# Kernel tuning notes

Hardware: AMD Instinct MI355X
Metric: run time of the kernel (lower is better)

The kernel has to match this reference:

```python
import jax, jax.numpy as jnp
import numpy as np

H = 64
L = 3
NG = 1024
# node types: 0 user, 1 card, 2 transaction, 3 merchant, 4 location, 5 device
N_NODES = [100000, 150000, 500000, 20000, 5000, 50000]
N_TX = N_NODES[2]
FEAT_DIMS = [8, 6, 12, 6, 5, 5]
NAMES = ["user", "card", "transaction", "merchant", "location", "device"]
# relation r -> (src_type, dst_type); order matches the HeteroConv dict:
# owns, made, at, in, using, followed_by, owned_by, made_with, receives, has, used_in, preceded
REL = [(0, 1), (1, 2), (2, 3), (2, 4), (2, 5), (2, 2), (1, 0), (2, 1), (3, 2), (4, 2), (5, 2), (2, 2)]
E_CNT = [150000, 500000, 500000, 500000, 500000, 500000, 150000, 500000, 500000, 500000, 500000, 500000]


def gat_conv(x_src, x_dst, src, dst, W, a_s, a_d, b, n_dst):
    # PyG GATConv, heads=1, shared src/dst linear (int in_channels), no self-loops (bipartite hetero)
    xs = x_src @ W  # [Ns, H]
    xd = x_dst @ W  # [Nd, H]
    e = jax.nn.leaky_relu((xs @ a_s)[src] + (xd @ a_d)[dst], 0.2)  # [E]
    m = jax.ops.segment_max(e, dst, num_segments=n_dst)
    m = jnp.where(jnp.isfinite(m), m, 0.0)
    p = jnp.exp(e - m[dst])
    s = jax.ops.segment_sum(p, dst, num_segments=n_dst)
    alpha = p / (s[dst] + 1e-16)
    out = jax.ops.segment_sum(alpha[:, None] * xs[src], dst, num_segments=n_dst)
    return out + b


def setup_inputs():
    key = jax.random.key(0)
    ks = iter(jax.random.split(key, 80))
    inp = {}
    for n, d, nm in zip(N_NODES, FEAT_DIMS, NAMES):
        inp["x_" + nm] = jax.random.normal(next(ks), (n, d), jnp.float32)
    for d, nm in zip(FEAT_DIMS, NAMES):
        inp["emb_" + nm + "_W"] = (jax.random.normal(next(ks), (d, H), jnp.float32) / np.sqrt(d)).astype(jnp.float32)
        inp["emb_" + nm + "_b"] = jnp.zeros((H,), jnp.float32)
    inp["gat_W"] = (jax.random.normal(next(ks), (L, 12, H, H), jnp.float32) / np.sqrt(H)).astype(jnp.float32)
    inp["gat_a_src"] = jax.random.normal(next(ks), (L, 12, H), jnp.float32) * 0.1
    inp["gat_a_dst"] = jax.random.normal(next(ks), (L, 12, H), jnp.float32) * 0.1
    inp["gat_b"] = jnp.zeros((L, 12, H), jnp.float32)
    inp["pool_W"] = (jax.random.normal(next(ks), (2 * H, H), jnp.float32) / np.sqrt(2 * H)).astype(jnp.float32)
    inp["pool_b"] = jnp.zeros((H,), jnp.float32)
    inp["cls_W1"] = (jax.random.normal(next(ks), (H, H), jnp.float32) / np.sqrt(H)).astype(jnp.float32)
    inp["cls_b1"] = jnp.zeros((H,), jnp.float32)
    inp["cls_W2"] = (jax.random.normal(next(ks), (H, 1), jnp.float32) / np.sqrt(H)).astype(jnp.float32)
    inp["cls_b2"] = jnp.zeros((1,), jnp.float32)
    for r, (s, d) in enumerate(REL):
        inp[f"e{r}_src"] = jax.random.randint(next(ks), (E_CNT[r],), 0, N_NODES[s])
        inp[f"e{r}_dst"] = jax.random.randint(next(ks), (E_CNT[r],), 0, N_NODES[d])
    inp["batch"] = jnp.sort(jax.random.randint(next(ks), (N_TX,), 0, NG))
    return inp


def reference(x_user, x_card, x_transaction, x_merchant, x_location, x_device,
              emb_user_W, emb_user_b, emb_card_W, emb_card_b,
              emb_transaction_W, emb_transaction_b, emb_merchant_W, emb_merchant_b,
              emb_location_W, emb_location_b, emb_device_W, emb_device_b,
              gat_W, gat_a_src, gat_a_dst, gat_b,
              pool_W, pool_b, cls_W1, cls_b1, cls_W2, cls_b2,
              e0_src, e0_dst, e1_src, e1_dst, e2_src, e2_dst, e3_src, e3_dst,
              e4_src, e4_dst, e5_src, e5_dst, e6_src, e6_dst, e7_src, e7_dst,
              e8_src, e8_dst, e9_src, e9_dst, e10_src, e10_dst, e11_src, e11_dst,
              batch):
    edges = [(e0_src, e0_dst), (e1_src, e1_dst), (e2_src, e2_dst), (e3_src, e3_dst),
             (e4_src, e4_dst), (e5_src, e5_dst), (e6_src, e6_dst), (e7_src, e7_dst),
             (e8_src, e8_dst), (e9_src, e9_dst), (e10_src, e10_dst), (e11_src, e11_dst)]
    x = [x_user @ emb_user_W + emb_user_b,
         x_card @ emb_card_W + emb_card_b,
         x_transaction @ emb_transaction_W + emb_transaction_b,
         x_merchant @ emb_merchant_W + emb_merchant_b,
         x_location @ emb_location_W + emb_location_b,
         x_device @ emb_device_W + emb_device_b]
    for l in range(L):
        agg = [jnp.zeros((n, H), x[0].dtype) for n in N_NODES]
        for r, (s, d) in enumerate(REL):  # HeteroConv default aggr='sum'
            agg[d] = agg[d] + gat_conv(x[s], x[d], edges[r][0], edges[r][1],
                                       gat_W[l, r], gat_a_src[l, r], gat_a_dst[l, r],
                                       gat_b[l, r], N_NODES[d])
        x = [jax.nn.relu(a) for a in agg]  # dropout(p=0.2) is identity in eval mode
    tx = x[2]
    cnt = jax.ops.segment_sum(jnp.ones((N_TX,), tx.dtype), batch, num_segments=NG)
    mean_pool = jax.ops.segment_sum(tx, batch, num_segments=NG) / jnp.maximum(cnt, 1.0)[:, None]
    max_pool = jax.ops.segment_max(tx, batch, num_segments=NG)
    max_pool = jnp.where(jnp.isfinite(max_pool), max_pool, 0.0)
    pooled = jnp.concatenate([mean_pool, max_pool], axis=1) @ pool_W + pool_b
    h = jax.nn.relu(tx @ cls_W1 + cls_b1)
    fraud_scores = jax.nn.sigmoid(h @ cls_W2 + cls_b2)
    return fraud_scores, pooled
```

## Files before the change

kernel.cpp:

```cpp
#include <hip/hip_runtime.h>
#include <hip/hip_bf16.h>

typedef unsigned int u32;
typedef unsigned short u16;
typedef _Float16 f16;
typedef float f32x4 __attribute__((ext_vector_type(4)));
typedef short bf16x8 __attribute__((ext_vector_type(8)));

#define CDIV(a,b) (((a)+(b)-1)/(b))

__device__ __forceinline__ float bf2f(u32 h){ return __uint_as_float(h<<16); }
__device__ __forceinline__ u16 f2bf(float f){
  u32 u=__float_as_uint(f);
  return (u16)((u + 0x7fffu + ((u>>16)&1u))>>16);
}
__device__ __forceinline__ u32 fenc(float f){
  u32 u=__float_as_uint(f);
  return (u&0x80000000u)?~u:(u|0x80000000u);
}
__device__ __forceinline__ float fdec2(u32 e){
  u32 u=(e&0x80000000u)?(e&0x7fffffffu):~e;
  return __uint_as_float(u);
}
__device__ __forceinline__ void unpack8(const u16* p, float* xr){
  uint4 v=*(const uint4*)p;
  xr[0]=bf2f(v.x&0xffffu); xr[1]=bf2f(v.x>>16);
  xr[2]=bf2f(v.y&0xffffu); xr[3]=bf2f(v.y>>16);
  xr[4]=bf2f(v.z&0xffffu); xr[5]=bf2f(v.z>>16);
  xr[6]=bf2f(v.w&0xffffu); xr[7]=bf2f(v.w>>16);
}
__device__ __forceinline__ int iclamp(int i, int n){
  unsigned u=(unsigned)i; return (u>=(unsigned)n)?0:i;
}

struct EdgeTab {
  const int* dst[12];
  const int* src[12];
  int seo[13];
  int rpo[13];
  int nd[12];
  int ns[12];
};

struct GTab {
  int nn[6]; int xo[6];
  int rst[12]; int rdt[12];
  int aso[12], ado[12], rpo[12], seo[12];
  int tord[6]; int bofs[7];
  int abofs[7];
  int nrel[6], rel[6][6];
  int nrole[6]; int rwv[6][12]; int rofs[6][12];
  int dszb;
};

__global__ void kdiag(float* out, int n, float v){
  int i=blockIdx.x*blockDim.x+threadIdx.x;
  if(i<n) out[i]=(i==0)?v:0.f;
}
__global__ void kzeroi(int* p, int n){
  int i=blockIdx.x*blockDim.x+threadIdx.x;
  if(i<n) p[i]=0;
}
__global__ void kbsum(const float* __restrict__ gb, float* __restrict__ bsum){
  int l=blockIdx.x/6, t=blockIdx.x%6, j=threadIdx.x;
  const int rd[12]={1,2,3,4,5,2,0,1,2,2,2,2};
  float a=0.f;
  #pragma unroll
  for(int r=0;r<12;++r) if(rd[r]==t) a += gb[(l*12+r)*64 + j];
  bsum[(l*6+t)*64 + j]=a;
}
__global__ void kwconv(const float* __restrict__ gw, u16* __restrict__ wt, int total){
  int o=blockIdx.x*blockDim.x+threadIdx.x;
  if(o>=total) return;
  int m=o>>12, rem=o&4095, j=rem>>6, k=rem&63;
  wt[o]=f2bf(gw[(m<<12)+(k<<6)+j]);
}
__global__ void kwv(const float* __restrict__ gw, const float* __restrict__ gas,
                    const float* __restrict__ gad, float* __restrict__ wv){
  int m=blockIdx.x;
  int lr=m>>1, role=m&1;
  int k=threadIdx.x;
  const float* a=(role?gad:gas)+(size_t)lr*64;
  const float* W=gw+(size_t)lr*4096;
  float acc=0.f;
  for(int j=0;j<64;++j) acc += W[k*64+j]*a[j];
  wv[(size_t)m*64+k]=acc;
}

__global__ void khistC(EdgeTab et, int* __restrict__ RP, int Etot, int c0, int c1){
  int i=blockIdx.x*blockDim.x+threadIdx.x;
  if(i>=Etot) return;
  int r=0;
  #pragma unroll
  for(int k=1;k<12;++k) r += (i>=et.seo[k]) ? 1 : 0;
  int e=i-et.seo[r];
  int rpidx=et.rpo[r]+iclamp(et.dst[r][e], et.nd[r]);
  if(rpidx>=c0 && rpidx<c1) atomicAdd(RP+rpidx,1);
}
__global__ void kscan1(const int* __restrict__ hist, int* __restrict__ rp, int* __restrict__ bsum, int N){
  __shared__ int lds[256];
  __shared__ int pref[256];
  int b=blockIdx.x, t=threadIdx.x;
  int base=b*4096+t*16;
  int v[16]; int s=0;
  #pragma unroll
  for(int k=0;k<16;++k){ int idx=base+k; v[k]=(idx<N)?hist[idx]:0; s+=v[k]; }
  lds[t]=s; __syncthreads();
  if(t==0){ int run=0; for(int i=0;i<256;++i){ pref[i]=run; run+=lds[i]; } bsum[b]=run; }
  __syncthreads();
  int run=pref[t];
  #pragma unroll
  for(int k=0;k<16;++k){ int idx=base+k; if(idx<N) rp[idx]=run; run+=v[k]; }
}
__global__ void kscan2b(int* bsum, int nb){
  __shared__ int lds[256], pref[256], tot;
  int t=threadIdx.x;
  int v[4]; int s=0;
  #pragma unroll
  for(int k=0;k<4;++k){ int idx=t*4+k; v[k]=(idx<nb)?bsum[idx]:0; s+=v[k]; }
  lds[t]=s; __syncthreads();
  if(t==0){ int run=0; for(int i=0;i<256;++i){ pref[i]=run; run+=lds[i]; } tot=run; }
  __syncthreads();
  int run=pref[t];
  #pragma unroll
  for(int k=0;k<4;++k){ int idx=t*4+k; if(idx<nb){ int x=v[k]; bsum[idx]=run; run+=x; } }
  if(t==0) bsum[nb]=tot;
}
__global__ void kscan3(int* __restrict__ rp, const int* __restrict__ bsum, int N){
  int i=blockIdx.x*blockDim.x+threadIdx.x;
  if(i<N) rp[i]+=bsum[i>>12];
}
__global__ void kscatterC(EdgeTab et, int* __restrict__ RP, int* __restrict__ SRCS,
                          int Etot, int c0, int c1){
  int i=blockIdx.x*blockDim.x+threadIdx.x;
  if(i>=Etot) return;
  int r=0;
  #pragma unroll
  for(int k=1;k<12;++k) r += (i>=et.seo[k]) ? 1 : 0;
  int e=i-et.seo[r];
  int rpidx=et.rpo[r]+iclamp(et.dst[r][e], et.nd[r]);
  if(rpidx>=c0 && rpidx<c1){
    int pos=atomicAdd(RP+rpidx,1);
    SRCS[pos]=iclamp(et.src[r][e], et.ns[r]);
  }
}

template<int D>
__global__ void kemb(const float* __restrict__ xin, const float* __restrict__ W,
                     const float* __restrict__ b, u16* __restrict__ xout, int N,
                     const float* __restrict__ WV0, f16* __restrict__ AA, GTab tab, int t){
  int n=blockIdx.x*blockDim.x+threadIdx.x;
  if(n>=N) return;
  float xr[D];
  #pragma unroll
  for(int k=0;k<D;++k) xr[k]=xin[(long)n*D+k];
  float o[64];
  u16* orow=xout+(long)n*64;
  #pragma unroll
  for(int j0=0;j0<64;j0+=8){
    #pragma unroll
    for(int jj=0;jj<8;++jj){
      float a=b[j0+jj];
      #pragma unroll
      for(int k=0;k<D;++k) a += xr[k]*W[k*64+j0+jj];
      o[j0+jj]=a;
    }
    uint4 pk;
    pk.x=(u32)f2bf(o[j0+0])|((u32)f2bf(o[j0+1])<<16);
    pk.y=(u32)f2bf(o[j0+2])|((u32)f2bf(o[j0+3])<<16);
    pk.z=(u32)f2bf(o[j0+4])|((u32)f2bf(o[j0+5])<<16);
    pk.w=(u32)f2bf(o[j0+6])|((u32)f2bf(o[j0+7])<<16);
    *(uint4*)(orow+j0)=pk;
  }
  int nr=tab.nrole[t];
  for(int ro=0;ro<nr;++ro){
    const float* wv=WV0+(size_t)tab.rwv[t][ro]*64;
    float acc=0.f;
    #pragma unroll
    for(int k=0;k<64;++k) acc += o[k]*wv[k];
    AA[tab.rofs[t][ro]+n]=(f16)acc;
  }
}

__global__ void kalphaM(const u16* __restrict__ X, const float* __restrict__ WVl,
                        f16* __restrict__ AA, GTab tab){
  __shared__ float wv[12*64];
  int b=blockIdx.x, tid=threadIdx.x;
  int ti=0;
  #pragma unroll
  for(int k=1;k<6;++k) ti += (b>=tab.abofs[k]) ? 1 : 0;
  int t=tab.tord[ti];
  int nr=tab.nrole[t];
  for(int i=tid;i<nr*64;i+=256){
    int ro=i>>6, j=i&63;
    wv[i]=WVl[tab.rwv[t][ro]*64+j];
  }
  __syncthreads();
  int nid=(b-tab.abofs[ti])*256+tid;
  if(nid>=tab.nn[t]) return;
  const u16* row=X+((long)tab.xo[t]+nid)*64;
  float xr[64];
  #pragma unroll
  for(int j=0;j<64;j+=8) unpack8(row+j,xr+j);
  for(int ro=0;ro<nr;++ro){
    float acc=0.f;
    #pragma unroll
    for(int k=0;k<64;++k) acc += xr[k]*wv[ro*64+k];
    AA[tab.rofs[t][ro]+nid]=(f16)acc;
  }
}

__global__ void kmg(const f16* __restrict__ AA, u32* __restrict__ MGl, GTab tab){
  const int NB=8;
  int b=blockIdx.x;
  int ro=b/NB, part=b%NB;
  int r=ro>>1, role=ro&1;
  int base,len;
  if(role==0){ base=tab.aso[r];           len=tab.nn[tab.rst[r]]; }
  else       { base=tab.dszb+tab.ado[r];  len=tab.nn[tab.rdt[r]]; }
  int i0=(int)((long)len*part/NB), i1=(int)((long)len*(part+1)/NB);
  float m=-3.4e38f;
  for(int i=i0+threadIdx.x;i<i1;i+=256) m=fmaxf(m,(float)AA[base+i]);
  #pragma unroll
  for(int off=32;off;off>>=1) m=fmaxf(m,__shfl_xor(m,off));
  __shared__ float red[4];
  if((threadIdx.x&63)==0) red[threadIdx.x>>6]=m;
  __syncthreads();
  if(threadIdx.x==0){
    float mm=fmaxf(fmaxf(red[0],red[1]),fmaxf(red[2],red[3]));
    atomicMax(MGl+ro,fenc(mm));
  }
}

#define LZ 0
#define LW 8192
__global__ void kfusedM2(const u16* __restrict__ Xc, u16* __restrict__ Xn,
                         const u16* __restrict__ WTl, const f16* __restrict__ AA,
                         const int* __restrict__ RP, const int* __restrict__ SRCS,
                         const float* __restrict__ BSl, const u32* __restrict__ MGl,
                         GTab tab){
  __shared__ char L[16384];
  int tid=threadIdx.x;
  int b=blockIdx.x;
  int ti=0;
  #pragma unroll
  for(int k=1;k<6;++k) ti += (b>=tab.bofs[k]) ? 1 : 0;
  int t=tab.tord[ti];
  int d0=(b-tab.bofs[ti])*64;
  int Nt=tab.nn[t];
  int nid=tid>>2, q=tid&3;
  int d=d0+nid;

  f32x4 acc[4];
  #pragma unroll
  for(int ct=0;ct<4;++ct){ acc[ct][0]=0.f; acc[ct][1]=0.f; acc[ct][2]=0.f; acc[ct][3]=0.f; }

  int nrel=tab.nrel[t];
  for(int ri=0;ri<nrel;++ri){
    int r=tab.rel[t][ri];
    float msum=fdec2(MGl[r*2])+fdec2(MGl[r*2+1]);
    float m = msum>=0.f? msum : 0.2f*msum;
    __syncthreads();
    {
      const uint4* s4=(const uint4*)(WTl+(size_t)r*4096);
      uint4 v0=s4[tid*2], v1=s4[tid*2+1];
      int b0=tid*32, j=b0>>7;
      *(uint4*)(L+LW+((b0   )^((j&7)<<4)))=v0;
      *(uint4*)(L+LW+((b0+16)^((j&7)<<4)))=v1;
    }
    float z[16];
    #pragma unroll
    for(int k=0;k<16;++k) z[k]=0.f;
    float sden=0.f;
    if(d<Nt){
      int b1=RP[tab.rpo[r]+d];
      int b0e= d? RP[tab.rpo[r]+d-1] : tab.seo[r];
      float adv=(float)AA[tab.dszb+tab.ado[r]+d];
      const u16* xbase=Xc+(long)tab.xo[tab.rst[r]]*64;
      const f16* asp=AA+tab.aso[r];
      int e=b0e;
      for(; e+1<b1; e+=2){
        int sr0=SRCS[e], sr1=SRCS[e+1];
        float ev0=(float)asp[sr0]+adv; ev0 = ev0>=0.f?ev0:0.2f*ev0;
        float ev1=(float)asp[sr1]+adv; ev1 = ev1>=0.f?ev1:0.2f*ev1;
        float p0=__expf(ev0-m), p1=__expf(ev1-m);
        const u16* rw0=xbase+(long)sr0*64+q*16;
        const u16* rw1=xbase+(long)sr1*64+q*16;
        uint4 a0=*(const uint4*)rw0;
        uint4 a1=*(const uint4*)(rw0+8);
        uint4 c0=*(const uint4*)rw1;
        uint4 c1=*(const uint4*)(rw1+8);
        sden+=p0+p1;
        float xr[8];
        unpack8((const u16*)&a0,xr);
        #pragma unroll
        for(int k=0;k<8;++k) z[k]+=p0*xr[k];
        unpack8((const u16*)&a1,xr);
        #pragma unroll
        for(int k=0;k<8;++k) z[8+k]+=p0*xr[k];
        unpack8((const u16*)&c0,xr);
        #pragma unroll
        for(int k=0;k<8;++k) z[k]+=p1*xr[k];
        unpack8((const u16*)&c1,xr);
        #pragma unroll
        for(int k=0;k<8;++k) z[8+k]+=p1*xr[k];
      }
      if(e<b1){
        int sr0=SRCS[e];
        float ev0=(float)asp[sr0]+adv; ev0 = ev0>=0.f?ev0:0.2f*ev0;
        float p0=__expf(ev0-m);
        const u16* rw0=xbase+(long)sr0*64+q*16;
        uint4 a0=*(const uint4*)rw0;
        uint4 a1=*(const uint4*)(rw0+8);
        sden+=p0;
        float xr[8];
        unpack8((const u16*)&a0,xr);
        #pragma unroll
        for(int k=0;k<8;++k) z[k]+=p0*xr[k];
        unpack8((const u16*)&a1,xr);
        #pragma unroll
        for(int k=0;k<8;++k) z[8+k]+=p0*xr[k];
      }
    }
    float inv=1.f/(sden+1e-16f);
    {
      uint4 p0,p1;
      p0.x=(u32)f2bf(z[0]*inv) |((u32)f2bf(z[1]*inv)<<16);
      p0.y=(u32)f2bf(z[2]*inv) |((u32)f2bf(z[3]*inv)<<16);
      p0.z=(u32)f2bf(z[4]*inv) |((u32)f2bf(z[5]*inv)<<16);
      p0.w=(u32)f2bf(z[6]*inv) |((u32)f2bf(z[7]*inv)<<16);
      p1.x=(u32)f2bf(z[8]*inv) |((u32)f2bf(z[9]*inv)<<16);
      p1.y=(u32)f2bf(z[10]*inv)|((u32)f2bf(z[11]*inv)<<16);
      p1.z=(u32)f2bf(z[12]*inv)|((u32)f2bf(z[13]*inv)<<16);
      p1.w=(u32)f2bf(z[14]*inv)|((u32)f2bf(z[15]*inv)<<16);
      int zb=nid*128+q*32;
      *(uint4*)(L+LZ+((zb   )^((nid&7)<<4)))=p0;
      *(uint4*)(L+LZ+((zb+16)^((nid&7)<<4)))=p1;
    }
    __syncthreads();
    {
      int w=tid>>6, l=tid&63;
      int nt=w*16;
      int arow=nt+(l&15);
      int kb=(l>>4)*8;
      #pragma unroll
      for(int ks=0;ks<64;ks+=32){
        int ab=arow*128+(ks+kb)*2;
        uint4 av=*(uint4*)(L+LZ+(ab^((arow&7)<<4)));
        bf16x8 af=*(bf16x8*)&av;
        #pragma unroll
        for(int ct=0;ct<4;++ct){
          int jrow=ct*16+(l&15);
          int bb=jrow*128+(ks+kb)*2;
          uint4 bv=*(uint4*)(L+LW+(bb^((jrow&7)<<4)));
          bf16x8 bfr=*(bf16x8*)&bv;
          acc[ct]=__builtin_amdgcn_mfma_f32_16x16x32_bf16(af,bfr,acc[ct],0,0,0);
        }
      }
    }
  }
  __syncthreads();
  {
    int w=tid>>6, l=tid&63;
    int nt=w*16;
    #pragma unroll
    for(int ct=0;ct<4;++ct){
      #pragma unroll
      for(int r4=0;r4<4;++r4){
        int crow=nt+(l>>4)*4+r4;
        int ccol=ct*16+(l&15);
        int cb=crow*256+ccol*4;
        *(float*)(L+(cb^((crow&7)<<4)))=acc[ct][r4];
      }
    }
  }
  __syncthreads();
  {
    int nn=tid>>2, cq=tid&3;
    if(d0+nn<Nt){
      float cv[16];
      #pragma unroll
      for(int p=0;p<4;++p){
        int cb=nn*256+cq*64+p*16;
        uint4 v=*(uint4*)(L+(cb^((nn&7)<<4)));
        const float* f=(const float*)&v;
        cv[p*4+0]=f[0]; cv[p*4+1]=f[1]; cv[p*4+2]=f[2]; cv[p*4+3]=f[3];
      }
      const float* bs=BSl+t*64+cq*16;
      u32 wd[8];
      #pragma unroll
      for(int i=0;i<8;++i){
        float lo=fmaxf(cv[2*i]  +bs[2*i],  0.f);
        float hi=fmaxf(cv[2*i+1]+bs[2*i+1],0.f);
        wd[i]=(u32)f2bf(lo)|((u32)f2bf(hi)<<16);
      }
      u16* orow=Xn+((long)tab.xo[t]+d0+nn)*64+cq*16;
      uint4 s0; s0.x=wd[0]; s0.y=wd[1]; s0.z=wd[2]; s0.w=wd[3];
      uint4 s1; s1.x=wd[4]; s1.y=wd[5]; s1.z=wd[6]; s1.w=wd[7];
      *(uint4*)orow=s0;
      *(uint4*)(orow+8)=s1;
    }
  }
}

__global__ void kcls(const u16* __restrict__ tx, const float* __restrict__ W1,
                     const float* __restrict__ b1, const float* __restrict__ W2,
                     const float* __restrict__ b2, float* __restrict__ out, int N){
  int n=blockIdx.x*blockDim.x+threadIdx.x;
  if(n>=N) return;
  const u16* row=tx+(long)n*64;
  float xr[64];
  #pragma unroll
  for(int j=0;j<64;j+=8) unpack8(row+j,xr+j);
  float acc2=0.f;
  for(int j=0;j<64;++j){
    float a=b1[j];
    #pragma unroll
    for(int k=0;k<64;++k) a += xr[k]*W1[k*64+j];
    a=fmaxf(a,0.f);
    acc2 += a*W2[j];
  }
  float zv=acc2+b2[0];
  out[n]=1.f/(1.f+__expf(-zv));
}

__global__ void kgrp(const int* __restrict__ batch, int* __restrict__ grp, int N){
  int g=blockIdx.x*blockDim.x+threadIdx.x;
  if(g>1024) return;
  if(g==1024){ grp[1024]=N; return; }
  int lo=0, hi=N;
  while(lo<hi){ int mid=(lo+hi)>>1; if(batch[mid]<g) lo=mid+1; else hi=mid; }
  grp[g]=lo;
}
__global__ void kpoolf(const u16* __restrict__ tx, const int* __restrict__ grp,
                       const float* __restrict__ pW, const float* __restrict__ pb,
                       float* __restrict__ out){
  __shared__ float S[256], M[256], V[128];
  int g=blockIdx.x, t=threadIdx.x, w=t>>6, j=t&63;
  int n0=grp[g], n1=grp[g+1];
  float s=0.f, m=-3.4e38f;
  for(int n=n0+w; n<n1; n+=4){
    float v=bf2f(tx[(long)n*64+j]);
    s+=v; m=fmaxf(m,v);
  }
  S[t]=s; M[t]=m; __syncthreads();
  if(t<64){
    float ss=S[t]+S[t+64]+S[t+128]+S[t+192];
    float mm=fmaxf(fmaxf(M[t],M[t+64]),fmaxf(M[t+128],M[t+192]));
    int cnt=n1-n0;
    V[t]=ss/fmaxf((float)cnt,1.f);
    V[64+t]=(cnt>0)?mm:0.f;
  }
  __syncthreads();
  if(t<64){
    float acc=pb[t];
    for(int k=0;k<128;++k) acc+=V[k]*pW[k*64+t];
    out[(long)g*64+t]=acc;
  }
}

extern "C" void kernel_launch(void* const* d_in, const int* in_sizes, int n_in,
                              void* d_out, int out_size, void* d_ws, size_t ws_size,
                              hipStream_t stream){
  const int   NN[6]={100000,150000,500000,20000,5000,50000};
  const long  XO[6]={0,100000,250000,750000,770000,775000};
  const int   RS[12]={0,1,2,2,2,2,1,2,3,4,5,2};
  const int   RD[12]={1,2,3,4,5,2,0,1,2,2,2,2};
  const int   EC[12]={150000,500000,500000,500000,500000,500000,150000,500000,500000,500000,500000,500000};

  const float* xin[6];  for(int t=0;t<6;++t) xin[t]=(const float*)d_in[t];
  const float* embW[6]; const float* embB[6];
  for(int t=0;t<6;++t){ embW[t]=(const float*)d_in[6+2*t]; embB[t]=(const float*)d_in[7+2*t]; }
  const float* gatW =(const float*)d_in[18];
  const float* gatAs=(const float*)d_in[19];
  const float* gatAd=(const float*)d_in[20];
  const float* gatB =(const float*)d_in[21];
  const float* poolW=(const float*)d_in[22];
  const float* poolB=(const float*)d_in[23];
  const float* W1=(const float*)d_in[24];
  const float* b1=(const float*)d_in[25];
  const float* W2=(const float*)d_in[26];
  const float* b2=(const float*)d_in[27];
  const int* esrc[12]; const int* edst[12];
  for(int r=0;r<12;++r){ esrc[r]=(const int*)d_in[28+2*r]; edst[r]=(const int*)d_in[29+2*r]; }
  const int* batch=(const int*)d_in[52];
  float* out=(float*)d_out;
  (void)in_sizes; (void)n_in;

  EdgeTab et;
  GTab tab;
  int rpo=0, seo=0, asz=0, dsz=0;
  for(int r=0;r<12;++r){
    et.dst[r]=edst[r]; et.src[r]=esrc[r];
    et.seo[r]=seo; et.rpo[r]=rpo;
    et.nd[r]=NN[RD[r]]; et.ns[r]=NN[RS[r]];
    tab.rst[r]=RS[r]; tab.rdt[r]=RD[r];
    tab.seo[r]=seo; tab.rpo[r]=rpo;
    tab.aso[r]=asz; tab.ado[r]=dsz;
    seo+=EC[r]; rpo+=NN[RD[r]]+1;
    asz+=NN[RS[r]]; dsz+=NN[RD[r]];
  }
  et.seo[12]=seo; et.rpo[12]=rpo;
  const int Etot=seo;
  const int RPtot=rpo;
  tab.dszb=asz;
  for(int t=0;t<6;++t){ tab.nn[t]=NN[t]; tab.xo[t]=(int)XO[t]; }
  const int TORD[6]={4,3,5,2,1,0};
  int bo=0, abo=0;
  for(int i=0;i<6;++i){
    int t=TORD[i];
    tab.tord[i]=t;
    tab.bofs[i]=bo;   bo+=CDIV(NN[t],64);
    tab.abofs[i]=abo; abo+=CDIV(NN[t],256);
  }
  tab.bofs[6]=bo; tab.abofs[6]=abo;
  for(int t=0;t<6;++t){ tab.nrel[t]=0; tab.nrole[t]=0; }
  for(int r=0;r<12;++r){
    int dt=RD[r];
    tab.rel[dt][tab.nrel[dt]++]=r;
    int st=RS[r];
    tab.rwv[st][tab.nrole[st]]=r*2+0;   tab.rofs[st][tab.nrole[st]++]=tab.aso[r];
    tab.rwv[dt][tab.nrole[dt]]=r*2+1;   tab.rofs[dt][tab.nrole[dt]++]=asz+tab.ado[r];
  }

  char* w=(char*)d_ws;
  size_t off=0;
  auto take=[&](size_t bytes)->void*{
    void* p=w+off; off+=(bytes+(size_t)255)&~(size_t)255; return p;
  };
  u16*   X1   =(u16*)  take(105600000);
  u16*   X2   =(u16*)  take(105600000);
  int*   RP   =(int*)  take((size_t)RPtot*4);
  int*   SRCS =(int*)  take((size_t)Etot*4);
  int*   BS   =(int*)  take(4096);
  f16*   AA   =(f16*)  take((size_t)(asz+dsz)*2);
  float* WV   =(float*)take(72*64*4);
  float* BSUM =(float*)take(4608);
  int*   GRP  =(int*)  take(4104);
  u16*   WT   =(u16*)  take(294912);
  u32*   MG   =(u32*)  take(288);
  size_t need=off;

  const int B=256;

  if(ws_size<need){
    kdiag<<<CDIV(out_size,B),B,0,stream>>>(out,out_size,(float)(ws_size>>20));
    return;
  }

  kwconv<<<CDIV(147456,B),B,0,stream>>>(gatW,WT,147456);
  kwv<<<72,64,0,stream>>>(gatW,gatAs,gatAd,WV);
  kbsum<<<18,64,0,stream>>>(gatB,BSUM);
  kzeroi<<<1,72,0,stream>>>((int*)MG,72);

  const int NCH=8;
  int CS=CDIV(RPtot,NCH);
  kzeroi<<<CDIV(RPtot,B),B,0,stream>>>(RP,RPtot);
  for(int c=0;c<NCH;++c){
    int c0=c*CS, c1=min(RPtot,c0+CS);
    khistC<<<CDIV(Etot,B),B,0,stream>>>(et,RP,Etot,c0,c1);
  }
  int nbs=CDIV(RPtot,4096);
  kscan1<<<nbs,256,0,stream>>>(RP,RP,BS,RPtot);
  kscan2b<<<1,256,0,stream>>>(BS,nbs);
  kscan3<<<CDIV(RPtot,B),B,0,stream>>>(RP,BS,RPtot);
  for(int c=0;c<NCH;++c){
    int c0=c*CS, c1=min(RPtot,c0+CS);
    kscatterC<<<CDIV(Etot,B),B,0,stream>>>(et,RP,SRCS,Etot,c0,c1);
  }

  kemb< 8><<<CDIV(NN[0],B),B,0,stream>>>(xin[0],embW[0],embB[0],X1+XO[0]*64,NN[0],WV,AA,tab,0);
  kemb< 6><<<CDIV(NN[1],B),B,0,stream>>>(xin[1],embW[1],embB[1],X1+XO[1]*64,NN[1],WV,AA,tab,1);
  kemb<12><<<CDIV(NN[2],B),B,0,stream>>>(xin[2],embW[2],embB[2],X1+XO[2]*64,NN[2],WV,AA,tab,2);
  kemb< 6><<<CDIV(NN[3],B),B,0,stream>>>(xin[3],embW[3],embB[3],X1+XO[3]*64,NN[3],WV,AA,tab,3);
  kemb< 5><<<CDIV(NN[4],B),B,0,stream>>>(xin[4],embW[4],embB[4],X1+XO[4]*64,NN[4],WV,AA,tab,4);
  kemb< 5><<<CDIV(NN[5],B),B,0,stream>>>(xin[5],embW[5],embB[5],X1+XO[5]*64,NN[5],WV,AA,tab,5);

  u16* Xc=X1; u16* Xn=X2;
  for(int l=0;l<3;++l){
    if(l>0) kalphaM<<<abo,256,0,stream>>>(Xc,WV+(size_t)l*1536,AA,tab);
    kmg<<<24*8,256,0,stream>>>(AA,MG+(size_t)l*24,tab);
    kfusedM2<<<bo,256,0,stream>>>(Xc,Xn,WT+(size_t)l*49152,AA,RP,SRCS,
                                  BSUM+(size_t)l*384,MG+(size_t)l*24,tab);
    u16* tmp=Xc; Xc=Xn; Xn=tmp;
  }

  kcls<<<CDIV(NN[2],B),B,0,stream>>>(Xc+XO[2]*64,W1,b1,W2,b2,out,NN[2]);

  kgrp<<<CDIV(1025,B),B,0,stream>>>(batch,GRP,NN[2]);
  kpoolf<<<1024,256,0,stream>>>(Xc+XO[2]*64,GRP,poolW,poolB,out+500000);
}
```

Baseline: 2.344 ms.

## Double-buffer relation gather in fused GAT kernel and collapse chunked CSR build

The fused GAT kernel now double-buffers its LDS for the aggregated features and relation weights. It gathers the next relation's softmax-weighted neighbour sum while the MFMA for the current relation runs, which cuts one barrier per relation. The CSR histogram and scatter passes drop from eight chunked launches each to a single full pass. The MG zeroing moves into the kwv kernel, removing one launch. LDS use doubles to 32 KB per block, which may lower occupancy. The unchunked scatter also loses the destination locality that chunking gave the atomics.

New measurement: 2.284 ms. -2.6%, faster.

```diff
diff --git a/kernel.cpp b/kernel.cpp
--- a/kernel.cpp
+++ b/kernel.cpp
@@ -76,10 +76,15 @@
   wt[o]=f2bf(gw[(m<<12)+(k<<6)+j]);
 }
 __global__ void kwv(const float* __restrict__ gw, const float* __restrict__ gas,
-                    const float* __restrict__ gad, float* __restrict__ wv){
+                    const float* __restrict__ gad, float* __restrict__ wv,
+                    u32* __restrict__ MG){
   int m=blockIdx.x;
   int lr=m>>1, role=m&1;
   int k=threadIdx.x;
+  if(k==0){
+    int l=lr/12, r=lr%12;
+    MG[l*24+r*2+role]=0u;
+  }
   const float* a=(role?gad:gas)+(size_t)lr*64;
   const float* W=gw+(size_t)lr*4096;
   float acc=0.f;
@@ -87,15 +92,15 @@
   wv[(size_t)m*64+k]=acc;
 }
 
-__global__ void khistC(EdgeTab et, int* __restrict__ RP, int Etot, int c0, int c1){
+__global__ void khistAll(EdgeTab et, int* __restrict__ RP, int Etot){
   int i=blockIdx.x*blockDim.x+threadIdx.x;
   if(i>=Etot) return;
   int r=0;
   #pragma unroll
   for(int k=1;k<12;++k) r += (i>=et.seo[k]) ? 1 : 0;
   int e=i-et.seo[r];
-  int rpidx=et.rpo[r]+iclamp(et.dst[r][e], et.nd[r]);
-  if(rpidx>=c0 && rpidx<c1) atomicAdd(RP+rpidx,1);
+  int d=iclamp(et.dst[r][e], et.nd[r]);
+  atomicAdd(RP+et.rpo[r]+d,1);
 }
 __global__ void kscan1(const int* __restrict__ hist, int* __restrict__ rp, int* __restrict__ bsum, int N){
   __shared__ int lds[256];
@@ -130,19 +135,16 @@
   int i=blockIdx.x*blockDim.x+threadIdx.x;
   if(i<N) rp[i]+=bsum[i>>12];
 }
-__global__ void kscatterC(EdgeTab et, int* __restrict__ RP, int* __restrict__ SRCS,
-                          int Etot, int c0, int c1){
+__global__ void kscatterAll(EdgeTab et, int* __restrict__ RP, int* __restrict__ SRCS, int Etot){
   int i=blockIdx.x*blockDim.x+threadIdx.x;
   if(i>=Etot) return;
   int r=0;
   #pragma unroll
   for(int k=1;k<12;++k) r += (i>=et.seo[k]) ? 1 : 0;
   int e=i-et.seo[r];
-  int rpidx=et.rpo[r]+iclamp(et.dst[r][e], et.nd[r]);
-  if(rpidx>=c0 && rpidx<c1){
-    int pos=atomicAdd(RP+rpidx,1);
-    SRCS[pos]=iclamp(et.src[r][e], et.ns[r]);
-  }
+  int d=iclamp(et.dst[r][e], et.nd[r]);
+  int pos=atomicAdd(RP+et.rpo[r]+d,1);
+  SRCS[pos]=iclamp(et.src[r][e], et.ns[r]);
 }
 
 template<int D>
@@ -232,14 +234,99 @@
   }
 }
 
-#define LZ 0
-#define LW 8192
+__device__ __forceinline__ void stage_wt(const u16* __restrict__ WTl, int r, int tid, char* wbuf){
+  const uint4* s4=(const uint4*)(WTl+(size_t)r*4096);
+  uint4 v0=s4[tid*2], v1=s4[tid*2+1];
+  int b0=tid*32, j=b0>>7;
+  *(uint4*)(wbuf+((b0   )^((j&7)<<4)))=v0;
+  *(uint4*)(wbuf+((b0+16)^((j&7)<<4)))=v1;
+}
+
+__device__ __forceinline__ void gather_z(int r, int d, int Nt, int nid, int q,
+                                         const f16* __restrict__ AA,
+                                         const int* __restrict__ RP,
+                                         const int* __restrict__ SRCS,
+                                         const u16* __restrict__ Xc,
+                                         const u32* __restrict__ MGl,
+                                         const GTab& tab, char* zbuf){
+  float msum=fdec2(MGl[r*2])+fdec2(MGl[r*2+1]);
+  float m = msum>=0.f? msum : 0.2f*msum;
+  float z[16];
+  #pragma unroll
+  for(int k=0;k<16;++k) z[k]=0.f;
+  float sden=0.f;
+  if(d<Nt){
+    int b1=RP[tab.rpo[r]+d];
+    int b0e= d? RP[tab.rpo[r]+d-1] : tab.seo[r];
+    float adv=(float)AA[tab.dszb+tab.ado[r]+d];
+    const u16* xbase=Xc+(long)tab.xo[tab.rst[r]]*64;
+    const f16* asp=AA+tab.aso[r];
+    int e=b0e;
+    for(; e+1<b1; e+=2){
+      int sr0=SRCS[e], sr1=SRCS[e+1];
+      float ev0=(float)asp[sr0]+adv; ev0 = ev0>=0.f?ev0:0.2f*ev0;
+      float ev1=(float)asp[sr1]+adv; ev1 = ev1>=0.f?ev1:0.2f*ev1;
+      float p0=__expf(ev0-m), p1=__expf(ev1-m);
+      const u16* rw0=xbase+(long)sr0*64+q*16;
+      const u16* rw1=xbase+(long)sr1*64+q*16;
+      uint4 a0=*(const uint4*)rw0;
+      uint4 a1=*(const uint4*)(rw0+8);
+      uint4 c0=*(const uint4*)rw1;
+      uint4 c1=*(const uint4*)(rw1+8);
+      sden+=p0+p1;
+      float xr[8];
+      unpack8((const u16*)&a0,xr);
+      #pragma unroll
+      for(int k=0;k<8;++k) z[k]+=p0*xr[k];
+      unpack8((const u16*)&a1,xr);
+      #pragma unroll
+      for(int k=0;k<8;++k) z[8+k]+=p0*xr[k];
+      unpack8((const u16*)&c0,xr);
+      #pragma unroll
+      for(int k=0;k<8;++k) z[k]+=p1*xr[k];
+      unpack8((const u16*)&c1,xr);
+      #pragma unroll
+      for(int k=0;k<8;++k) z[8+k]+=p1*xr[k];
+    }
+    if(e<b1){
+      int sr0=SRCS[e];
+      float ev0=(float)asp[sr0]+adv; ev0 = ev0>=0.f?ev0:0.2f*ev0;
+      float p0=__expf(ev0-m);
+      const u16* rw0=xbase+(long)sr0*64+q*16;
+      uint4 a0=*(const uint4*)rw0;
+      uint4 a1=*(const uint4*)(rw0+8);
+      sden+=p0;
+      float xr[8];
+      unpack8((const u16*)&a0,xr);
+      #pragma unroll
+      for(int k=0;k<8;++k) z[k]+=p0*xr[k];
+      unpack8((const u16*)&a1,xr);
+      #pragma unroll
+      for(int k=0;k<8;++k) z[8+k]+=p0*xr[k];
+    }
+  }
+  float inv=1.f/(sden+1e-16f);
+  uint4 p0,p1;
+  p0.x=(u32)f2bf(z[0]*inv) |((u32)f2bf(z[1]*inv)<<16);
+  p0.y=(u32)f2bf(z[2]*inv) |((u32)f2bf(z[3]*inv)<<16);
+  p0.z=(u32)f2bf(z[4]*inv) |((u32)f2bf(z[5]*inv)<<16);
+  p0.w=(u32)f2bf(z[6]*inv) |((u32)f2bf(z[7]*inv)<<16);
+  p1.x=(u32)f2bf(z[8]*inv) |((u32)f2bf(z[9]*inv)<<16);
+  p1.y=(u32)f2bf(z[10]*inv)|((u32)f2bf(z[11]*inv)<<16);
+  p1.z=(u32)f2bf(z[12]*inv)|((u32)f2bf(z[13]*inv)<<16);
+  p1.w=(u32)f2bf(z[14]*inv)|((u32)f2bf(z[15]*inv)<<16);
+  int zb=nid*128+q*32;
+  *(uint4*)(zbuf+((zb   )^((nid&7)<<4)))=p0;
+  *(uint4*)(zbuf+((zb+16)^((nid&7)<<4)))=p1;
+}
+
 __global__ void kfusedM2(const u16* __restrict__ Xc, u16* __restrict__ Xn,
                          const u16* __restrict__ WTl, const f16* __restrict__ AA,
                          const int* __restrict__ RP, const int* __restrict__ SRCS,
                          const float* __restrict__ BSl, const u32* __restrict__ MGl,
                          GTab tab){
-  __shared__ char L[16384];
+  __shared__ char Lraw[32768];
+  char* L=(char*)Lraw;
   int tid=threadIdx.x;
   int b=blockIdx.x;
   int ti=0;
@@ -256,88 +343,18 @@
   for(int ct=0;ct<4;++ct){ acc[ct][0]=0.f; acc[ct][1]=0.f; acc[ct][2]=0.f; acc[ct][3]=0.f; }
 
   int nrel=tab.nrel[t];
+  gather_z(tab.rel[t][0],d,Nt,nid,q,AA,RP,SRCS,Xc,MGl,tab,L);
+  stage_wt(WTl,tab.rel[t][0],tid,L+16384);
+  __syncthreads();
+
   for(int ri=0;ri<nrel;++ri){
-    int r=tab.rel[t][ri];
-    float msum=fdec2(MGl[r*2])+fdec2(MGl[r*2+1]);
-    float m = msum>=0.f? msum : 0.2f*msum;
-    __syncthreads();
-    {
-      const uint4* s4=(const uint4*)(WTl+(size_t)r*4096);
-      uint4 v0=s4[tid*2], v1=s4[tid*2+1];
-      int b0=tid*32, j=b0>>7;
-      *(uint4*)(L+LW+((b0   )^((j&7)<<4)))=v0;
-      *(uint4*)(L+LW+((b0+16)^((j&7)<<4)))=v1;
+    int zcur = (ri&1)? 8192 : 0;
+    int wcur = 16384 + zcur;
+    if(ri+1<nrel){
+      int znxt = (ri&1)? 0 : 8192;
+      gather_z(tab.rel[t][ri+1],d,Nt,nid,q,AA,RP,SRCS,Xc,MGl,tab,L+znxt);
+      stage_wt(WTl,tab.rel[t][ri+1],tid,L+16384+znxt);
     }
-    float z[16];
-    #pragma unroll
-    for(int k=0;k<16;++k) z[k]=0.f;
-    float sden=0.f;
-    if(d<Nt){
-      int b1=RP[tab.rpo[r]+d];
-      int b0e= d? RP[tab.rpo[r]+d-1] : tab.seo[r];
-      float adv=(float)AA[tab.dszb+tab.ado[r]+d];
-      const u16* xbase=Xc+(long)tab.xo[tab.rst[r]]*64;
-      const f16* asp=AA+tab.aso[r];
-      int e=b0e;
-      for(; e+1<b1; e+=2){
-        int sr0=SRCS[e], sr1=SRCS[e+1];
-        float ev0=(float)asp[sr0]+adv; ev0 = ev0>=0.f?ev0:0.2f*ev0;
-        float ev1=(float)asp[sr1]+adv; ev1 = ev1>=0.f?ev1:0.2f*ev1;
-        float p0=__expf(ev0-m), p1=__expf(ev1-m);
-        const u16* rw0=xbase+(long)sr0*64+q*16;
-        const u16* rw1=xbase+(long)sr1*64+q*16;
-        uint4 a0=*(const uint4*)rw0;
-        uint4 a1=*(const uint4*)(rw0+8);
-        uint4 c0=*(const uint4*)rw1;
-        uint4 c1=*(const uint4*)(rw1+8);
-        sden+=p0+p1;
-        float xr[8];
-        unpack8((const u16*)&a0,xr);
-        #pragma unroll
-        for(int k=0;k<8;++k) z[k]+=p0*xr[k];
-        unpack8((const u16*)&a1,xr);
-        #pragma unroll
-        for(int k=0;k<8;++k) z[8+k]+=p0*xr[k];
-        unpack8((const u16*)&c0,xr);
-        #pragma unroll
-        for(int k=0;k<8;++k) z[k]+=p1*xr[k];
-        unpack8((const u16*)&c1,xr);
-        #pragma unroll
-        for(int k=0;k<8;++k) z[8+k]+=p1*xr[k];
-      }
-      if(e<b1){
-        int sr0=SRCS[e];
-        float ev0=(float)asp[sr0]+adv; ev0 = ev0>=0.f?ev0:0.2f*ev0;
-        float p0=__expf(ev0-m);
-        const u16* rw0=xbase+(long)sr0*64+q*16;
-        uint4 a0=*(const uint4*)rw0;
-        uint4 a1=*(const uint4*)(rw0+8);
-        sden+=p0;
-        float xr[8];
-        unpack8((const u16*)&a0,xr);
-        #pragma unroll
-        for(int k=0;k<8;++k) z[k]+=p0*xr[k];
-        unpack8((const u16*)&a1,xr);
-        #pragma unroll
-        for(int k=0;k<8;++k) z[8+k]+=p0*xr[k];
-      }
-    }
-    float inv=1.f/(sden+1e-16f);
-    {
-      uint4 p0,p1;
-      p0.x=(u32)f2bf(z[0]*inv) |((u32)f2bf(z[1]*inv)<<16);
-      p0.y=(u32)f2bf(z[2]*inv) |((u32)f2bf(z[3]*inv)<<16);
-      p0.z=(u32)f2bf(z[4]*inv) |((u32)f2bf(z[5]*inv)<<16);
-      p0.w=(u32)f2bf(z[6]*inv) |((u32)f2bf(z[7]*inv)<<16);
-      p1.x=(u32)f2bf(z[8]*inv) |((u32)f2bf(z[9]*inv)<<16);
-      p1.y=(u32)f2bf(z[10]*inv)|((u32)f2bf(z[11]*inv)<<16);
-      p1.z=(u32)f2bf(z[12]*inv)|((u32)f2bf(z[13]*inv)<<16);
-      p1.w=(u32)f2bf(z[14]*inv)|((u32)f2bf(z[15]*inv)<<16);
-      int zb=nid*128+q*32;
-      *(uint4*)(L+LZ+((zb   )^((nid&7)<<4)))=p0;
-      *(uint4*)(L+LZ+((zb+16)^((nid&7)<<4)))=p1;
-    }
-    __syncthreads();
     {
       int w=tid>>6, l=tid&63;
       int nt=w*16;
@@ -346,20 +363,21 @@
       #pragma unroll
       for(int ks=0;ks<64;ks+=32){
         int ab=arow*128+(ks+kb)*2;
-        uint4 av=*(uint4*)(L+LZ+(ab^((arow&7)<<4)));
+        uint4 av=*(uint4*)(L+zcur+(ab^((arow&7)<<4)));
         bf16x8 af=*(bf16x8*)&av;
         #pragma unroll
         for(int ct=0;ct<4;++ct){
           int jrow=ct*16+(l&15);
           int bb=jrow*128+(ks+kb)*2;
-          uint4 bv=*(uint4*)(L+LW+(bb^((jrow&7)<<4)));
+          uint4 bv=*(uint4*)(L+wcur+(bb^((jrow&7)<<4)));
           bf16x8 bfr=*(bf16x8*)&bv;
           acc[ct]=__builtin_amdgcn_mfma_f32_16x16x32_bf16(af,bfr,acc[ct],0,0,0);
         }
       }
     }
-  }
-  __syncthreads();
+    __syncthreads();
+  }
+
   {
     int w=tid>>6, l=tid&63;
     int nt=w*16;
@@ -549,25 +567,16 @@
   }
 
   kwconv<<<CDIV(147456,B),B,0,stream>>>(gatW,WT,147456);
-  kwv<<<72,64,0,stream>>>(gatW,gatAs,gatAd,WV);
+  kwv<<<72,64,0,stream>>>(gatW,gatAs,gatAd,WV,MG);
   kbsum<<<18,64,0,stream>>>(gatB,BSUM);
-  kzeroi<<<1,72,0,stream>>>((int*)MG,72);
-
-  const int NCH=8;
-  int CS=CDIV(RPtot,NCH);
+
+  int nbs=CDIV(RPtot,4096);
   kzeroi<<<CDIV(RPtot,B),B,0,stream>>>(RP,RPtot);
-  for(int c=0;c<NCH;++c){
-    int c0=c*CS, c1=min(RPtot,c0+CS);
-    khistC<<<CDIV(Etot,B),B,0,stream>>>(et,RP,Etot,c0,c1);
-  }
-  int nbs=CDIV(RPtot,4096);
+  khistAll<<<CDIV(Etot,B),B,0,stream>>>(et,RP,Etot);
   kscan1<<<nbs,256,0,stream>>>(RP,RP,BS,RPtot);
   kscan2b<<<1,256,0,stream>>>(BS,nbs);
   kscan3<<<CDIV(RPtot,B),B,0,stream>>>(RP,BS,RPtot);
-  for(int c=0;c<NCH;++c){
-    int c0=c*CS, c1=min(RPtot,c0+CS);
-    kscatterC<<<CDIV(Etot,B),B,0,stream>>>(et,RP,SRCS,Etot,c0,c1);
-  }
+  kscatterAll<<<CDIV(Etot,B),B,0,stream>>>(et,RP,SRCS,Etot);
 
   kemb< 8><<<CDIV(NN[0],B),B,0,stream>>>(xin[0],embW[0],embB[0],X1+XO[0]*64,NN[0],WV,AA,tab,0);
   kemb< 6><<<CDIV(NN[1],B),B,0,stream>>>(xin[1],embW[1],embB[1],X1+XO[1]*64,NN[1],WV,AA,tab,1);
```
